# Kernel tuning notes

Measured on AMD Instinct MI355X. Metric: run time of the kernel, lower is better.

Reference implementation:

```python
import jax, jax.numpy as jnp
import numpy as np

EPS = 1e-5
SLOPE = 0.2

def _inorm(x):
    # InstanceNorm2d with affine=False on [B, C, N, 1]: normalize over spatial N per (b, c).
    mu = jnp.mean(x, axis=-1, keepdims=True)
    var = jnp.var(x, axis=-1, keepdims=True)  # biased variance, matches torch InstanceNorm
    return (x - mu) * jax.lax.rsqrt(var + EPS)

def _lrelu(x):
    return jnp.where(x >= 0, x, SLOPE * x)

def _block(W, x):
    # 1x1 conv (channel matmul) -> instance norm -> leaky relu; x: [B, Cin, N]
    return _lrelu(_inorm(jnp.einsum('oc,bcn->bon', W, x)))

def setup_inputs() -> dict:
    key = jax.random.key(0)
    k1, k2, k3, k4, k5 = jax.random.split(key, 5)
    B, C, N = 8, 256, 2048
    feat = jax.random.normal(k1, (B, C, N), dtype=jnp.float32)
    W1 = jax.random.normal(k2, (2 * C, C), dtype=jnp.float32) * (1.0 / np.sqrt(C))
    W2 = jax.random.normal(k3, (2 * C, C), dtype=jnp.float32) * (1.0 / np.sqrt(C))
    W3 = jax.random.normal(k4, (2 * C, C), dtype=jnp.float32) * (1.0 / np.sqrt(C))
    W4 = jax.random.normal(k5, (C, 2 * C), dtype=jnp.float32) * (1.0 / np.sqrt(2 * C))
    return {"feat": feat, "W1": W1, "W2": W2, "W3": W3, "W4": W4}

def reference(feat, W1, W2, W3, W4):
    # feat: [B, C, N]
    x1 = _block(W1, feat)  # [B, 2C, N]
    x2 = _block(W2, feat)  # [B, 2C, N]
    x3 = _block(W3, feat)  # [B, 2C, N]
    # query_key: x1^T @ x2 -> [B, N, N]
    qk = jnp.einsum('bcn,bcm->bnm', x1, x2)
    # x3 @ qk -> [B, 2C, N]; offset attention: subtract from x1
    x4 = x1 - jnp.einsum('bcn,bnm->bcm', x3, qk)
    out = _block(W4, x4)  # [B, C, N]
    return out
```

## Files before the change

### kernel.cpp

```cpp
#include <hip/hip_runtime.h>
#include <stdint.h>


#define LRELU_SLOPE 0.2f
#define EPS_IN 1e-5f

typedef __attribute__((ext_vector_type(8))) short short8v;
typedef __attribute__((ext_vector_type(4))) float f32x4;

__device__ __forceinline__ unsigned short f2bf(float f) {
    unsigned int u = __builtin_bit_cast(unsigned int, f);
    u = (u + 0x7fffu + ((u >> 16) & 1u)) >> 16;
    return (unsigned short)u;
}
__device__ __forceinline__ float bf2f(unsigned short h) {
    return __builtin_bit_cast(float, (unsigned int)h << 16);
}

typedef const __attribute__((address_space(1))) unsigned int* as1_uint_ptr;
typedef __attribute__((address_space(3))) unsigned int* as3_uint_ptr;

#define GLL16(g, l) __builtin_amdgcn_global_load_lds( \
    (as1_uint_ptr)(const void*)(g), (as3_uint_ptr)(void*)(l), 16, 0, 0)

enum { EP_F32 = 0, EP_BF16 = 1, EP_SUB_T_SPLIT = 2, EP_BF16_STATS = 3 };

template<int BM, int BN, int EP>
__global__ __launch_bounds__(256)
void gemm_tn(const unsigned short* __restrict__ A, const unsigned short* __restrict__ B,
             const unsigned short* __restrict__ Dm, void* __restrict__ Cv,
             float2* __restrict__ part,
             int K, int lda, int ldb, int ldd, int ldc,
             int64_t sA, int64_t sB, int64_t sD, int64_t sC)
{
    constexpr int FM = BM / 32, FN = BN / 32;
    const int bz = blockIdx.z;
    A += sA * bz;
    B += sB * bz;

    const int i0 = blockIdx.y * BM;
    const int j0 = blockIdx.x * BN;

    __shared__ __align__(16) unsigned short As[BM * 32];
    __shared__ __align__(16) unsigned short Bs[BN * 32];

    const int t = threadIdx.x;
    const int w = t >> 6, l = t & 63;
    const int wr = w >> 1, wc = w & 1;

    f32x4 acc[FM][FN];
#pragma unroll
    for (int fm = 0; fm < FM; ++fm)
#pragma unroll
        for (int fn = 0; fn < FN; ++fn)
            acc[fm][fn] = (f32x4){0.f, 0.f, 0.f, 0.f};

    for (int k0 = 0; k0 < K; k0 += 32) {
        __syncthreads();
#pragma unroll
        for (int q = 0; q < BM / 64; ++q) {
            const int seg = w * (BM / 64) + q;
            const int row = seg * 16 + (l >> 2);
            GLL16(A + (size_t)(i0 + row) * lda + k0 + (l & 3) * 8, &As[seg * 512]);
        }
#pragma unroll
        for (int q = 0; q < BN / 64; ++q) {
            const int seg = w * (BN / 64) + q;
            const int row = seg * 16 + (l >> 2);
            GLL16(B + (size_t)(j0 + row) * ldb + k0 + (l & 3) * 8, &Bs[seg * 512]);
        }
        asm volatile("s_waitcnt vmcnt(0)" ::: "memory");
        __syncthreads();

        short8v a[FM], b[FN];
#pragma unroll
        for (int fm = 0; fm < FM; ++fm)
            a[fm] = *(const short8v*)&As[(wr * (BM / 2) + fm * 16 + (l & 15)) * 32 + (l >> 4) * 8];
#pragma unroll
        for (int fn = 0; fn < FN; ++fn)
            b[fn] = *(const short8v*)&Bs[(wc * (BN / 2) + fn * 16 + (l & 15)) * 32 + (l >> 4) * 8];
#pragma unroll
        for (int fm = 0; fm < FM; ++fm)
#pragma unroll
            for (int fn = 0; fn < FN; ++fn)
                acc[fm][fn] = __builtin_amdgcn_mfma_f32_16x16x32_bf16(a[fm], b[fn], acc[fm][fn], 0, 0, 0);
    }

    const int cr4 = (l >> 4) * 4;
    const int cc = l & 15;

    if constexpr (EP == EP_F32) {
        float* C = (float*)Cv + sC * bz;
#pragma unroll
        for (int fm = 0; fm < FM; ++fm)
#pragma unroll
            for (int fn = 0; fn < FN; ++fn)
#pragma unroll
                for (int r = 0; r < 4; ++r)
                    C[(size_t)(i0 + wr * (BM / 2) + fm * 16 + cr4 + r) * ldc +
                      (j0 + wc * (BN / 2) + fn * 16 + cc)] = acc[fm][fn][r];
    } else if constexpr (EP == EP_BF16) {
        unsigned short* C = (unsigned short*)Cv + sC * bz;
#pragma unroll
        for (int fm = 0; fm < FM; ++fm)
#pragma unroll
            for (int fn = 0; fn < FN; ++fn)
#pragma unroll
                for (int r = 0; r < 4; ++r)
                    C[(size_t)(i0 + wr * (BM / 2) + fm * 16 + cr4 + r) * ldc +
                      (j0 + wc * (BN / 2) + fn * 16 + cc)] = f2bf(acc[fm][fn][r]);
    } else if constexpr (EP == EP_SUB_T_SPLIT) {
        const unsigned short* D = Dm + sD * bz;
        unsigned short* C = (unsigned short*)Cv + sC * bz;
#pragma unroll
        for (int fm = 0; fm < FM; ++fm) {
            const int grow0 = i0 + wr * (BM / 2) + fm * 16 + cr4;
#pragma unroll
            for (int fn = 0; fn < FN; ++fn) {
                const int gcol = j0 + wc * (BN / 2) + fn * 16 + cc;
                ushort4 hi4, lo4;
#pragma unroll
                for (int r = 0; r < 4; ++r) {
                    const float sv = bf2f(D[(size_t)(grow0 + r) * ldd + gcol]) - acc[fm][fn][r];
                    const unsigned short h = f2bf(sv);
                    ((unsigned short*)&hi4)[r] = h;
                    ((unsigned short*)&lo4)[r] = f2bf(sv - bf2f(h));
                }
                *(ushort4*)&C[(size_t)gcol * ldc + grow0] = hi4;
                *(ushort4*)&C[(size_t)gcol * ldc + (ldc >> 1) + grow0] = lo4;
            }
        }
    } else {
        unsigned short* C = (unsigned short*)Cv + sC * bz;
        __shared__ float2 wp[2][BM];
#pragma unroll
        for (int fm = 0; fm < FM; ++fm) {
#pragma unroll
            for (int r = 0; r < 4; ++r) {
                float s = 0.f, q = 0.f;
#pragma unroll
                for (int fn = 0; fn < FN; ++fn) {
                    const float v = acc[fm][fn][r];
                    s += v; q += v * v;
                    C[(size_t)(i0 + wr * (BM / 2) + fm * 16 + cr4 + r) * ldc +
                      (j0 + wc * (BN / 2) + fn * 16 + cc)] = f2bf(v);
                }
#pragma unroll
                for (int m = 1; m < 16; m <<= 1) {
                    s += __shfl_xor(s, m, 64);
                    q += __shfl_xor(q, m, 64);
                }
                if ((l & 15) == 0)
                    wp[wc][wr * (BM / 2) + fm * 16 + cr4 + r] = make_float2(s, q);
            }
        }
        __syncthreads();
        if (t < BM) {
            const float2 p0 = wp[0][t], p1 = wp[1][t];
            part[(size_t)(bz * 1536 + i0 + t) * gridDim.x + blockIdx.x] =
                make_float2(p0.x + p1.x, p0.y + p1.y);
        }
    }
}

__global__ __launch_bounds__(256)
void reduce_stats(const float2* __restrict__ part, float2* __restrict__ stats)
{
    const int row = blockIdx.x * 256 + threadIdx.x;
    float S = 0.f, Q = 0.f;
#pragma unroll
    for (int j = 0; j < 16; ++j) {
        const float2 p = part[(size_t)row * 16 + j];
        S += p.x; Q += p.y;
    }
    const float mu = S * (1.0f / 2048.0f);
    const float var = Q * (1.0f / 2048.0f) - mu * mu;
    stats[row] = make_float2(mu, rsqrtf(var + EPS_IN));
}

__device__ __forceinline__ uint4 norm8(uint4 v, float2 st)
{
    const unsigned int wd[4] = {v.x, v.y, v.z, v.w};
    unsigned int o[4];
#pragma unroll
    for (int i = 0; i < 4; ++i) {
        float a = __builtin_bit_cast(float, wd[i] << 16);
        float b = __builtin_bit_cast(float, wd[i] & 0xffff0000u);
        a = (a - st.x) * st.y; a = a >= 0.f ? a : LRELU_SLOPE * a;
        b = (b - st.x) * st.y; b = b >= 0.f ? b : LRELU_SLOPE * b;
        o[i] = (unsigned int)f2bf(a) | ((unsigned int)f2bf(b) << 16);
    }
    return make_uint4(o[0], o[1], o[2], o[3]);
}

__global__ __launch_bounds__(256)
void norm12(const unsigned short* __restrict__ ybf, const float2* __restrict__ stats,
            unsigned short* __restrict__ x1n3)
{
    const int bz = blockIdx.y;
    const int x = blockIdx.x;
    const int src = (x < 512) ? x : (x + 512);
    const float2 st = stats[bz * 1536 + src];
    const uint4 v = ((const uint4*)(ybf + (size_t)bz * 3145728 + (size_t)src * 2048))[threadIdx.x];
    ((uint4*)(x1n3 + (size_t)bz * 2097152 + (size_t)x * 2048))[threadIdx.x] = norm8(v, st);
}

__global__ __launch_bounds__(256)
void transpose_norm_x2(const unsigned short* __restrict__ ybf,
                       const float2* __restrict__ stats,
                       unsigned short* __restrict__ x2T)
{
    __shared__ __align__(16) unsigned short tile[64][68];
    const int t = threadIdx.x, bz = blockIdx.z;
    const unsigned short* in = ybf + (size_t)bz * 3145728 + (size_t)512 * 2048;
    unsigned short* outp = x2T + (size_t)bz * 1048576;
    const int r0 = blockIdx.y * 64, c0 = blockIdx.x * 64;
    const int ir = t >> 4, ic = (t & 15) * 4;

#pragma unroll
    for (int q = 0; q < 4; ++q) {
        const int rr = q * 16 + ir;
        const float2 st = stats[bz * 1536 + 512 + r0 + rr];
        const ushort4 v = *(const ushort4*)&in[(size_t)(r0 + rr) * 2048 + c0 + ic];
        const unsigned short vv[4] = {v.x, v.y, v.z, v.w};
#pragma unroll
        for (int j = 0; j < 4; ++j) {
            float e = (bf2f(vv[j]) - st.x) * st.y;
            e = e >= 0.f ? e : LRELU_SLOPE * e;
            tile[rr][ic + j] = f2bf(e);
        }
    }
    __syncthreads();

    const int n = t & 63, kc = (t >> 6) * 16;
    unsigned short* op = outp + (size_t)(c0 + n) * 512 + r0 + kc;
    unsigned int wo[8];
#pragma unroll
    for (int i = 0; i < 8; ++i)
        wo[i] = (unsigned int)tile[kc + 2 * i][n] | ((unsigned int)tile[kc + 2 * i + 1][n] << 16);
    *(uint4*)op       = make_uint4(wo[0], wo[1], wo[2], wo[3]);
    *(uint4*)(op + 8) = make_uint4(wo[4], wo[5], wo[6], wo[7]);
}

__global__ __launch_bounds__(256)
void transpose_feat(const float* __restrict__ in, unsigned short* __restrict__ out)
{
    __shared__ __align__(16) unsigned short tile[64][68];
    const int t = threadIdx.x, bz = blockIdx.z;
    const float* ip0 = in + (size_t)bz * 524288;
    unsigned short* outp = out + (size_t)bz * 524288;
    const int r0 = blockIdx.y * 64, c0 = blockIdx.x * 64;
    const int ir = t >> 4, ic = (t & 15) * 4;

#pragma unroll
    for (int q = 0; q < 4; ++q) {
        const int rr = q * 16 + ir;
        const float4 v = *(const float4*)&ip0[(size_t)(r0 + rr) * 2048 + c0 + ic];
        tile[rr][ic + 0] = f2bf(v.x);
        tile[rr][ic + 1] = f2bf(v.y);
        tile[rr][ic + 2] = f2bf(v.z);
        tile[rr][ic + 3] = f2bf(v.w);
    }
    __syncthreads();

    const int n = t & 63, kc = (t >> 6) * 16;
    unsigned short* op = outp + (size_t)(c0 + n) * 256 + r0 + kc;
    unsigned int wo[8];
#pragma unroll
    for (int i = 0; i < 8; ++i)
        wo[i] = (unsigned int)tile[kc + 2 * i][n] | ((unsigned int)tile[kc + 2 * i + 1][n] << 16);
    *(uint4*)op       = make_uint4(wo[0], wo[1], wo[2], wo[3]);
    *(uint4*)(op + 8) = make_uint4(wo[4], wo[5], wo[6], wo[7]);
}

__global__ __launch_bounds__(256)
void row_norm_lrelu(const float* __restrict__ in, float* __restrict__ out)
{
    const size_t row = blockIdx.x;
    const float4* p = (const float4*)(in + row * 2048);
    float4* q = (float4*)(out + row * 2048);
    const int t = threadIdx.x;

    float4 v0 = p[t];
    float4 v1 = p[t + 256];

    float s  = v0.x + v0.y + v0.z + v0.w + v1.x + v1.y + v1.z + v1.w;
    float ss = v0.x * v0.x + v0.y * v0.y + v0.z * v0.z + v0.w * v0.w +
               v1.x * v1.x + v1.y * v1.y + v1.z * v1.z + v1.w * v1.w;
#pragma unroll
    for (int off = 32; off > 0; off >>= 1) {
        s  += __shfl_down(s, off, 64);
        ss += __shfl_down(ss, off, 64);
    }
    __shared__ float red[10];
    const int wid = t >> 6;
    if ((t & 63) == 0) { red[wid] = s; red[4 + wid] = ss; }
    __syncthreads();
    if (t == 0) {
        const float S  = red[0] + red[1] + red[2] + red[3];
        const float SS = red[4] + red[5] + red[6] + red[7];
        const float mu = S * (1.0f / 2048.0f);
        const float var = SS * (1.0f / 2048.0f) - mu * mu;
        red[8] = mu;
        red[9] = rsqrtf(var + EPS_IN);
    }
    __syncthreads();
    const float mu = red[8], rs = red[9];
#define NRM(x) { float e = ((x) - mu) * rs; (x) = (e >= 0.0f) ? e : LRELU_SLOPE * e; }
    NRM(v0.x) NRM(v0.y) NRM(v0.z) NRM(v0.w)
    NRM(v1.x) NRM(v1.y) NRM(v1.z) NRM(v1.w)
#undef NRM
    q[t] = v0;
    q[t + 256] = v1;
}

__global__ __launch_bounds__(256)
void cast_weights(const float* __restrict__ W1, const float* __restrict__ W2,
                  const float* __restrict__ W3, const float* __restrict__ W4,
                  unsigned short* __restrict__ Wcatb, unsigned short* __restrict__ W4cat)
{
    const int wsel = blockIdx.x >> 7;
    const int local = ((blockIdx.x & 127) * 256 + threadIdx.x) * 4;
    const float* src = (wsel == 0) ? W1 : (wsel == 1) ? W2 : (wsel == 2) ? W3 : W4;
    const float4 v = *(const float4*)(src + local);
    const ushort4 pk = make_ushort4(f2bf(v.x), f2bf(v.y), f2bf(v.z), f2bf(v.w));
    if (wsel < 3) {
        *(ushort4*)(Wcatb + (size_t)wsel * 131072 + local) = pk;
    } else {
        const int o = local >> 9, c = local & 511;
        *(ushort4*)(W4cat + (size_t)o * 1024 + c)       = pk;
        *(ushort4*)(W4cat + (size_t)o * 1024 + 512 + c) = pk;
    }
}

extern "C" void kernel_launch(void* const* d_in, const int* in_sizes, int n_in,
                              void* d_out, int out_size, void* d_ws, size_t ws_size,
                              hipStream_t stream)
{
    const float* feat = (const float*)d_in[0];
    const float* W1   = (const float*)d_in[1];
    const float* W2   = (const float*)d_in[2];
    const float* W3   = (const float*)d_in[3];
    const float* W4   = (const float*)d_in[4];
    float* out = (float*)d_out;

    char* w = (char*)d_ws;
    unsigned short* ybf   = (unsigned short*)(w + 0);
    unsigned short* x4Ts  = (unsigned short*)(w + 0);
    float*          z     = (float*)(w + 33554432);
    unsigned short* featT = (unsigned short*)(w + 50331648);
    unsigned short* x2T   = (unsigned short*)(w + 58720256);
    unsigned short* x1n3  = (unsigned short*)(w + 75497472);
    unsigned short* Amb   = (unsigned short*)(w + 109051904);
    unsigned short* Wcatb = (unsigned short*)(w + 113246208);
    unsigned short* W4cat = (unsigned short*)(w + 114032640);
    float2*         part1 = (float2*)(w + 114556928);
    float2*         stats = (float2*)(w + 116129792);

    cast_weights<<<512, 256, 0, stream>>>(W1, W2, W3, W4, Wcatb, W4cat);

    transpose_feat<<<dim3(32, 4, 8), 256, 0, stream>>>(feat, featT);

    gemm_tn<128, 128, EP_BF16_STATS><<<dim3(16, 12, 8), 256, 0, stream>>>(
        Wcatb, featT, nullptr, ybf, part1,
        256, 256, 256, 0, 2048, 0, 524288, 0, 3145728);

    reduce_stats<<<48, 256, 0, stream>>>(part1, stats);

    transpose_norm_x2<<<dim3(32, 8, 8), 256, 0, stream>>>(ybf, stats, x2T);
    norm12<<<dim3(1024, 8), 256, 0, stream>>>(ybf, stats, x1n3);

    gemm_tn<64, 64, EP_BF16><<<dim3(8, 8, 8), 256, 0, stream>>>(
        x1n3 + 1048576 , x1n3 , nullptr, Amb, nullptr,
        2048, 2048, 2048, 0, 512, 2097152, 2097152, 0, 262144);

    gemm_tn<128, 128, EP_SUB_T_SPLIT><<<dim3(16, 4, 8), 256, 0, stream>>>(
        Amb, x2T, x1n3, x4Ts, nullptr,
        512, 512, 512, 2048, 1024, 262144, 1048576, 2097152, 2097152);

    gemm_tn<128, 64, EP_F32><<<dim3(32, 2, 8), 256, 0, stream>>>(
        W4cat, x4Ts, nullptr, z, nullptr,
        1024, 1024, 1024, 0, 2048, 0, 2097152, 0, 524288);

    row_norm_lrelu<<<2048, 256, 0, stream>>>(z, out);
}
```

Baseline: 224.2 us.

## Double-buffer GEMM LDS tiles and merge prep and norm kernels

The bf16 MFMA GEMM now keeps two LDS buffers per operand. It issues the global-to-LDS loads for the next K tile before running the MFMAs on the current one, so load latency can overlap compute, with one barrier per iteration. Separately, weight casting and the feat transpose are merged into one prep launch, and the x2 transpose-normalize and x1/x3 normalize kernels are merged into one normx launch, to cut launch overhead and tail gaps. The explicit vmcnt wait before the barrier was removed, so correctness relies on the compiler inserting waits for the LDS DMA. If it inserts a full vmcnt(0) before the LDS reads, the overlap is lost. LDS use per block also doubles.

```diff
diff --git a/kernel.cpp b/kernel.cpp
--- a/kernel.cpp
+++ b/kernel.cpp
@@ -41,12 +41,13 @@
     const int i0 = blockIdx.y * BM;
     const int j0 = blockIdx.x * BN;
 
-    __shared__ __align__(16) unsigned short As[BM * 32];
-    __shared__ __align__(16) unsigned short Bs[BN * 32];
+    __shared__ __align__(16) unsigned short As[2][BM * 32];
+    __shared__ __align__(16) unsigned short Bs[2][BN * 32];
 
     const int t = threadIdx.x;
     const int w = t >> 6, l = t & 63;
     const int wr = w >> 1, wc = w & 1;
+    const int srow = l >> 2, skq = (l & 3) * 8;
 
     f32x4 acc[FM][FN];
 #pragma unroll
@@ -55,35 +56,48 @@
         for (int fn = 0; fn < FN; ++fn)
             acc[fm][fn] = (f32x4){0.f, 0.f, 0.f, 0.f};
 
-    for (int k0 = 0; k0 < K; k0 += 32) {
-        __syncthreads();
-#pragma unroll
-        for (int q = 0; q < BM / 64; ++q) {
-            const int seg = w * (BM / 64) + q;
-            const int row = seg * 16 + (l >> 2);
-            GLL16(A + (size_t)(i0 + row) * lda + k0 + (l & 3) * 8, &As[seg * 512]);
-        }
-#pragma unroll
-        for (int q = 0; q < BN / 64; ++q) {
-            const int seg = w * (BN / 64) + q;
-            const int row = seg * 16 + (l >> 2);
-            GLL16(B + (size_t)(j0 + row) * ldb + k0 + (l & 3) * 8, &Bs[seg * 512]);
-        }
-        asm volatile("s_waitcnt vmcnt(0)" ::: "memory");
-        __syncthreads();
-
+    const int NT = K / 32;
+
+#pragma unroll
+    for (int q = 0; q < BM / 64; ++q) {
+        const int seg = w * (BM / 64) + q;
+        GLL16(A + (size_t)(i0 + seg * 16 + srow) * lda + skq, &As[0][seg * 512]);
+    }
+#pragma unroll
+    for (int q = 0; q < BN / 64; ++q) {
+        const int seg = w * (BN / 64) + q;
+        GLL16(B + (size_t)(j0 + seg * 16 + srow) * ldb + skq, &Bs[0][seg * 512]);
+    }
+    __syncthreads();
+
+    for (int tt = 0; tt < NT; ++tt) {
+        const int cur = tt & 1;
+        if (tt + 1 < NT) {
+            const int k0 = (tt + 1) * 32;
+#pragma unroll
+            for (int q = 0; q < BM / 64; ++q) {
+                const int seg = w * (BM / 64) + q;
+                GLL16(A + (size_t)(i0 + seg * 16 + srow) * lda + k0 + skq, &As[cur ^ 1][seg * 512]);
+            }
+#pragma unroll
+            for (int q = 0; q < BN / 64; ++q) {
+                const int seg = w * (BN / 64) + q;
+                GLL16(B + (size_t)(j0 + seg * 16 + srow) * ldb + k0 + skq, &Bs[cur ^ 1][seg * 512]);
+            }
+        }
         short8v a[FM], b[FN];
 #pragma unroll
         for (int fm = 0; fm < FM; ++fm)
-            a[fm] = *(const short8v*)&As[(wr * (BM / 2) + fm * 16 + (l & 15)) * 32 + (l >> 4) * 8];
+            a[fm] = *(const short8v*)&As[cur][(wr * (BM / 2) + fm * 16 + (l & 15)) * 32 + (l >> 4) * 8];
 #pragma unroll
         for (int fn = 0; fn < FN; ++fn)
-            b[fn] = *(const short8v*)&Bs[(wc * (BN / 2) + fn * 16 + (l & 15)) * 32 + (l >> 4) * 8];
+            b[fn] = *(const short8v*)&Bs[cur][(wc * (BN / 2) + fn * 16 + (l & 15)) * 32 + (l >> 4) * 8];
 #pragma unroll
         for (int fm = 0; fm < FM; ++fm)
 #pragma unroll
             for (int fn = 0; fn < FN; ++fn)
                 acc[fm][fn] = __builtin_amdgcn_mfma_f32_16x16x32_bf16(a[fm], b[fn], acc[fm][fn], 0, 0, 0);
+        __syncthreads();
     }
 
     const int cr4 = (l >> 4) * 4;
@@ -194,83 +208,98 @@
 }
 
 __global__ __launch_bounds__(256)
-void norm12(const unsigned short* __restrict__ ybf, const float2* __restrict__ stats,
-            unsigned short* __restrict__ x1n3)
-{
-    const int bz = blockIdx.y;
-    const int x = blockIdx.x;
-    const int src = (x < 512) ? x : (x + 512);
-    const float2 st = stats[bz * 1536 + src];
-    const uint4 v = ((const uint4*)(ybf + (size_t)bz * 3145728 + (size_t)src * 2048))[threadIdx.x];
-    ((uint4*)(x1n3 + (size_t)bz * 2097152 + (size_t)x * 2048))[threadIdx.x] = norm8(v, st);
-}
-
-__global__ __launch_bounds__(256)
-void transpose_norm_x2(const unsigned short* __restrict__ ybf,
-                       const float2* __restrict__ stats,
-                       unsigned short* __restrict__ x2T)
-{
-    __shared__ __align__(16) unsigned short tile[64][68];
-    const int t = threadIdx.x, bz = blockIdx.z;
-    const unsigned short* in = ybf + (size_t)bz * 3145728 + (size_t)512 * 2048;
-    unsigned short* outp = x2T + (size_t)bz * 1048576;
-    const int r0 = blockIdx.y * 64, c0 = blockIdx.x * 64;
-    const int ir = t >> 4, ic = (t & 15) * 4;
-
-#pragma unroll
-    for (int q = 0; q < 4; ++q) {
-        const int rr = q * 16 + ir;
-        const float2 st = stats[bz * 1536 + 512 + r0 + rr];
-        const ushort4 v = *(const ushort4*)&in[(size_t)(r0 + rr) * 2048 + c0 + ic];
-        const unsigned short vv[4] = {v.x, v.y, v.z, v.w};
-#pragma unroll
-        for (int j = 0; j < 4; ++j) {
-            float e = (bf2f(vv[j]) - st.x) * st.y;
-            e = e >= 0.f ? e : LRELU_SLOPE * e;
-            tile[rr][ic + j] = f2bf(e);
-        }
-    }
-    __syncthreads();
-
-    const int n = t & 63, kc = (t >> 6) * 16;
-    unsigned short* op = outp + (size_t)(c0 + n) * 512 + r0 + kc;
-    unsigned int wo[8];
-#pragma unroll
-    for (int i = 0; i < 8; ++i)
-        wo[i] = (unsigned int)tile[kc + 2 * i][n] | ((unsigned int)tile[kc + 2 * i + 1][n] << 16);
-    *(uint4*)op       = make_uint4(wo[0], wo[1], wo[2], wo[3]);
-    *(uint4*)(op + 8) = make_uint4(wo[4], wo[5], wo[6], wo[7]);
-}
-
-__global__ __launch_bounds__(256)
-void transpose_feat(const float* __restrict__ in, unsigned short* __restrict__ out)
-{
-    __shared__ __align__(16) unsigned short tile[64][68];
-    const int t = threadIdx.x, bz = blockIdx.z;
-    const float* ip0 = in + (size_t)bz * 524288;
-    unsigned short* outp = out + (size_t)bz * 524288;
-    const int r0 = blockIdx.y * 64, c0 = blockIdx.x * 64;
-    const int ir = t >> 4, ic = (t & 15) * 4;
-
-#pragma unroll
-    for (int q = 0; q < 4; ++q) {
-        const int rr = q * 16 + ir;
-        const float4 v = *(const float4*)&ip0[(size_t)(r0 + rr) * 2048 + c0 + ic];
-        tile[rr][ic + 0] = f2bf(v.x);
-        tile[rr][ic + 1] = f2bf(v.y);
-        tile[rr][ic + 2] = f2bf(v.z);
-        tile[rr][ic + 3] = f2bf(v.w);
-    }
-    __syncthreads();
-
-    const int n = t & 63, kc = (t >> 6) * 16;
-    unsigned short* op = outp + (size_t)(c0 + n) * 256 + r0 + kc;
-    unsigned int wo[8];
-#pragma unroll
-    for (int i = 0; i < 8; ++i)
-        wo[i] = (unsigned int)tile[kc + 2 * i][n] | ((unsigned int)tile[kc + 2 * i + 1][n] << 16);
-    *(uint4*)op       = make_uint4(wo[0], wo[1], wo[2], wo[3]);
-    *(uint4*)(op + 8) = make_uint4(wo[4], wo[5], wo[6], wo[7]);
+void normx(const unsigned short* __restrict__ ybf, const float2* __restrict__ stats,
+           unsigned short* __restrict__ x2T, unsigned short* __restrict__ x1n3)
+{
+    const int b = blockIdx.x;
+    const int t = threadIdx.x;
+    if (b < 2048) {
+        __shared__ __align__(16) unsigned short tile[64][68];
+        const int bx = b & 31, by = (b >> 5) & 7, bz = b >> 8;
+        const unsigned short* in = ybf + (size_t)bz * 3145728 + (size_t)512 * 2048;
+        unsigned short* outp = x2T + (size_t)bz * 1048576;
+        const int r0 = by * 64, c0 = bx * 64;
+        const int ir = t >> 4, ic = (t & 15) * 4;
+#pragma unroll
+        for (int q = 0; q < 4; ++q) {
+            const int rr = q * 16 + ir;
+            const float2 st = stats[bz * 1536 + 512 + r0 + rr];
+            const ushort4 v = *(const ushort4*)&in[(size_t)(r0 + rr) * 2048 + c0 + ic];
+            const unsigned short vv[4] = {v.x, v.y, v.z, v.w};
+#pragma unroll
+            for (int j = 0; j < 4; ++j) {
+                float e = (bf2f(vv[j]) - st.x) * st.y;
+                e = e >= 0.f ? e : LRELU_SLOPE * e;
+                tile[rr][ic + j] = f2bf(e);
+            }
+        }
+        __syncthreads();
+        const int n = t & 63, kc = (t >> 6) * 16;
+        unsigned short* op = outp + (size_t)(c0 + n) * 512 + r0 + kc;
+        unsigned int wo[8];
+#pragma unroll
+        for (int i = 0; i < 8; ++i)
+            wo[i] = (unsigned int)tile[kc + 2 * i][n] | ((unsigned int)tile[kc + 2 * i + 1][n] << 16);
+        *(uint4*)op       = make_uint4(wo[0], wo[1], wo[2], wo[3]);
+        *(uint4*)(op + 8) = make_uint4(wo[4], wo[5], wo[6], wo[7]);
+    } else {
+        const int r = b - 2048;
+        const int x = r & 1023, bz = r >> 10;
+        const int src = (x < 512) ? x : (x + 512);
+        const float2 st = stats[bz * 1536 + src];
+        const uint4 v = ((const uint4*)(ybf + (size_t)bz * 3145728 + (size_t)src * 2048))[t];
+        ((uint4*)(x1n3 + (size_t)bz * 2097152 + (size_t)x * 2048))[t] = norm8(v, st);
+    }
+}
+
+__global__ __launch_bounds__(256)
+void prep(const float* __restrict__ W1, const float* __restrict__ W2,
+          const float* __restrict__ W3, const float* __restrict__ W4,
+          unsigned short* __restrict__ Wcatb, unsigned short* __restrict__ W4cat,
+          const float* __restrict__ feat, unsigned short* __restrict__ featT)
+{
+    const int b = blockIdx.x;
+    const int t = threadIdx.x;
+    if (b < 512) {
+        const int wsel = b >> 7;
+        const int local = ((b & 127) * 256 + t) * 4;
+        const float* src = (wsel == 0) ? W1 : (wsel == 1) ? W2 : (wsel == 2) ? W3 : W4;
+        const float4 v = *(const float4*)(src + local);
+        const ushort4 pk = make_ushort4(f2bf(v.x), f2bf(v.y), f2bf(v.z), f2bf(v.w));
+        if (wsel < 3) {
+            *(ushort4*)(Wcatb + (size_t)wsel * 131072 + local) = pk;
+        } else {
+            const int o = local >> 9, c = local & 511;
+            *(ushort4*)(W4cat + (size_t)o * 1024 + c)       = pk;
+            *(ushort4*)(W4cat + (size_t)o * 1024 + 512 + c) = pk;
+        }
+    } else {
+        __shared__ __align__(16) unsigned short tile[64][68];
+        const int r = b - 512;
+        const int bx = r & 31, by = (r >> 5) & 3, bz = r >> 7;
+        const float* ip0 = feat + (size_t)bz * 524288;
+        unsigned short* outp = featT + (size_t)bz * 524288;
+        const int r0 = by * 64, c0 = bx * 64;
+        const int ir = t >> 4, ic = (t & 15) * 4;
+#pragma unroll
+        for (int q = 0; q < 4; ++q) {
+            const int rr = q * 16 + ir;
+            const float4 v = *(const float4*)&ip0[(size_t)(r0 + rr) * 2048 + c0 + ic];
+            tile[rr][ic + 0] = f2bf(v.x);
+            tile[rr][ic + 1] = f2bf(v.y);
+            tile[rr][ic + 2] = f2bf(v.z);
+            tile[rr][ic + 3] = f2bf(v.w);
+        }
+        __syncthreads();
+        const int n = t & 63, kc = (t >> 6) * 16;
+        unsigned short* op = outp + (size_t)(c0 + n) * 256 + r0 + kc;
+        unsigned int wo[8];
+#pragma unroll
+        for (int i = 0; i < 8; ++i)
+            wo[i] = (unsigned int)tile[kc + 2 * i][n] | ((unsigned int)tile[kc + 2 * i + 1][n] << 16);
+        *(uint4*)op       = make_uint4(wo[0], wo[1], wo[2], wo[3]);
+        *(uint4*)(op + 8) = make_uint4(wo[4], wo[5], wo[6], wo[7]);
+    }
 }
 
 __global__ __launch_bounds__(256)
@@ -312,25 +341,6 @@
 #undef NRM
     q[t] = v0;
     q[t + 256] = v1;
-}
-
-__global__ __launch_bounds__(256)
-void cast_weights(const float* __restrict__ W1, const float* __restrict__ W2,
-                  const float* __restrict__ W3, const float* __restrict__ W4,
-                  unsigned short* __restrict__ Wcatb, unsigned short* __restrict__ W4cat)
-{
-    const int wsel = blockIdx.x >> 7;
-    const int local = ((blockIdx.x & 127) * 256 + threadIdx.x) * 4;
-    const float* src = (wsel == 0) ? W1 : (wsel == 1) ? W2 : (wsel == 2) ? W3 : W4;
-    const float4 v = *(const float4*)(src + local);
-    const ushort4 pk = make_ushort4(f2bf(v.x), f2bf(v.y), f2bf(v.z), f2bf(v.w));
-    if (wsel < 3) {
-        *(ushort4*)(Wcatb + (size_t)wsel * 131072 + local) = pk;
-    } else {
-        const int o = local >> 9, c = local & 511;
-        *(ushort4*)(W4cat + (size_t)o * 1024 + c)       = pk;
-        *(ushort4*)(W4cat + (size_t)o * 1024 + 512 + c) = pk;
-    }
 }
 
 extern "C" void kernel_launch(void* const* d_in, const int* in_sizes, int n_in,
@@ -357,9 +367,7 @@
     float2*         part1 = (float2*)(w + 114556928);
     float2*         stats = (float2*)(w + 116129792);
 
-    cast_weights<<<512, 256, 0, stream>>>(W1, W2, W3, W4, Wcatb, W4cat);
-
-    transpose_feat<<<dim3(32, 4, 8), 256, 0, stream>>>(feat, featT);
+    prep<<<1536, 256, 0, stream>>>(W1, W2, W3, W4, Wcatb, W4cat, feat, featT);
 
     gemm_tn<128, 128, EP_BF16_STATS><<<dim3(16, 12, 8), 256, 0, stream>>>(
         Wcatb, featT, nullptr, ybf, part1,
@@ -367,8 +375,7 @@
 
     reduce_stats<<<48, 256, 0, stream>>>(part1, stats);
 
-    transpose_norm_x2<<<dim3(32, 8, 8), 256, 0, stream>>>(ybf, stats, x2T);
-    norm12<<<dim3(1024, 8), 256, 0, stream>>>(ybf, stats, x1n3);
+    normx<<<10240, 256, 0, stream>>>(ybf, stats, x2T, x1n3);
 
     gemm_tn<64, 64, EP_BF16><<<dim3(8, 8, 8), 256, 0, stream>>>(
         x1n3 + 1048576 , x1n3 , nullptr, Amb, nullptr,
```

After: 210.4 us. 1.07x faster.
